# Kernel tuning notes

Hardware: AMD Instinct MI355X
Metric: run time of the kernel (lower is better)

## Reference

```python
import jax, jax.numpy as jnp
import numpy as np

# Structural metadata (constants): 3 node types, 4 edge types, 2 HGT layers.
T, R, L = 3, 4, 2
H_HID, HEADS, OUT = 256, 8, 128
D = H_HID // HEADS  # per-head dim = 32
SRC_T = (0, 1, 1, 1)  # (author->paper, paper->author, paper->paper, paper->venue)
DST_T = (1, 0, 1, 2)
LN_EPS = 1e-5


def _segment_softmax(logits, seg, n):
    # logits: [E, heads]; softmax over edges sharing the same destination node
    m = jax.ops.segment_max(logits, seg, num_segments=n)
    e = jnp.exp(logits - m[seg])
    s = jax.ops.segment_sum(e, seg, num_segments=n)
    return e / s[seg]


def setup_inputs() -> dict:
    key = jax.random.key(0)
    ks = iter(jax.random.split(key, 64))
    N, E, FIN = 20000, 60000, 128

    def nrm(shape, scale):
        return jax.random.normal(next(ks), shape, jnp.float32) * scale

    return dict(
        x=jax.random.normal(next(ks), (T, N, FIN), jnp.float32),
        edge_index=jax.random.randint(next(ks), (R, 2, E), 0, N),
        Win=nrm((T, FIN, H_HID), 0.05),
        b_in=jnp.zeros((T, H_HID), jnp.float32),
        Wk=nrm((L, T, H_HID, H_HID), 0.05), bk=jnp.zeros((L, T, H_HID), jnp.float32),
        Wq=nrm((L, T, H_HID, H_HID), 0.05), bq=jnp.zeros((L, T, H_HID), jnp.float32),
        Wv=nrm((L, T, H_HID, H_HID), 0.05), bv=jnp.zeros((L, T, H_HID), jnp.float32),
        Wa=nrm((L, T, H_HID, H_HID), 0.05), ba=jnp.zeros((L, T, H_HID), jnp.float32),
        skip=jnp.ones((L, T), jnp.float32),
        a_rel=nrm((L, R, HEADS, D, D), 0.1),
        m_rel=nrm((L, R, HEADS, D, D), 0.1),
        p_rel=jnp.ones((L, R, HEADS), jnp.float32),
        ln_g=jnp.ones((L, T, H_HID), jnp.float32),
        ln_b=jnp.zeros((L, T, H_HID), jnp.float32),
        Wout=nrm((H_HID, OUT), 0.05),
        bout=jnp.zeros((OUT,), jnp.float32),
    )


def reference(x, edge_index, Win, b_in, Wk, bk, Wq, bq, Wv, bv, Wa, ba,
              skip, a_rel, m_rel, p_rel, ln_g, ln_b, Wout, bout):
    N = x.shape[1]
    inv_sqrt_d = jnp.float32(1.0 / np.sqrt(D))
    # Input projection + ReLU (dropout = identity in eval mode)
    h = jax.nn.relu(jnp.einsum('tnf,tfh->tnh', x, Win) + b_in[:, None, :])

    for l in range(L):
        res = h
        # Per-node-type k/q/v projections, reshaped to heads
        k = (jnp.einsum('tnh,tho->tno', h, Wk[l]) + bk[l][:, None]).reshape(T, N, HEADS, D)
        q = (jnp.einsum('tnh,tho->tno', h, Wq[l]) + bq[l][:, None]).reshape(T, N, HEADS, D)
        v = (jnp.einsum('tnh,tho->tno', h, Wv[l]) + bv[l][:, None]).reshape(T, N, HEADS, D)

        agg = jnp.zeros((T, N, HEADS, D), h.dtype)
        for r in range(R):
            st, dt = SRC_T[r], DST_T[r]
            src, dst = edge_index[r, 0], edge_index[r, 1]
            # Per-edge-type relation transforms on source k/v
            k_r = jnp.einsum('nhd,hde->nhe', k[st], a_rel[l, r])
            v_r = jnp.einsum('nhd,hde->nhe', v[st], m_rel[l, r])
            kj = k_r[src]          # [E, heads, d]
            vj = v_r[src]
            qi = q[dt][dst]
            logits = (qi * kj).sum(-1) * p_rel[l, r] * inv_sqrt_d  # [E, heads]
            alpha = _segment_softmax(logits, dst, N)
            msg = vj * alpha[..., None]
            agg = agg.at[dt].add(jax.ops.segment_sum(msg, dst, num_segments=N))

        # Type-specific output linear after exact GELU, gated skip (in==out dims)
        o = jax.nn.gelu(agg.reshape(T, N, H_HID), approximate=False)
        o = jnp.einsum('tnh,tho->tno', o, Wa[l]) + ba[l][:, None]
        beta = jax.nn.sigmoid(skip[l])[:, None, None]
        h = beta * o + (1.0 - beta) * h

        # Model-level residual + LayerNorm + ReLU (dropout = identity)
        h = h + res
        mu = h.mean(-1, keepdims=True)
        var = ((h - mu) ** 2).mean(-1, keepdims=True)
        h = (h - mu) * jax.lax.rsqrt(var + LN_EPS) * ln_g[l][:, None] + ln_b[l][:, None]
        h = jax.nn.relu(h)

    # Shared output projection; outputs stacked over node types: [T, N, OUT]
    return jnp.einsum('tnh,ho->tno', h, Wout) + bout
```

## Files before the change

kernel.cpp:

```cpp
#include <hip/hip_runtime.h>
#include <math.h>

#define T_ 3
#define R_ 4
#define L_ 2
#define H_ 256
#define HEADS_ 8
#define D_ 32
#define FIN_ 128
#define OUT_ 128

typedef unsigned short bf16_t;
typedef __attribute__((ext_vector_type(8))) short bf16x8;
typedef __attribute__((ext_vector_type(4))) float f32x4;

__device__ __forceinline__ float bf2f(bf16_t h) {
    return __uint_as_float(((unsigned)h) << 16);
}
__device__ __forceinline__ bf16_t f2bf(float f) {
    unsigned u = __float_as_uint(f);
    u += 0x7FFFu + ((u >> 16) & 1u);
    return (bf16_t)(u >> 16);
}
__device__ __forceinline__ float gelu_exact(float x) {
    return 0.5f * x * (1.0f + erff(x * 0.70710678118654752440f));
}

__global__ void zero_kernel(unsigned* __restrict__ p, long n) {
    long i = (long)blockIdx.x * blockDim.x + threadIdx.x;
    long stride = (long)gridDim.x * blockDim.x;
    for (; i < n; i += stride) p[i] = 0u;
}

__global__ __launch_bounds__(256) void transconv_kernel(
    const float* __restrict__ in, bf16_t* __restrict__ out, int Rr, int Cc)
{
    __shared__ float Ls[64][65];
    const int tid = threadIdx.x;
    const long base = (long)blockIdx.z * Rr * Cc;
    const int r0 = blockIdx.y * 64, c0 = blockIdx.x * 64;
    #pragma unroll
    for (int i = 0; i < 16; ++i) {
        int e = tid + i * 256; int row = e >> 6, col = e & 63;
        Ls[row][col] = in[base + (long)(r0 + row) * Cc + c0 + col];
    }
    __syncthreads();
    #pragma unroll
    for (int i = 0; i < 16; ++i) {
        int e = tid + i * 256; int row = e >> 6, col = e & 63;
        out[base + (long)(c0 + row) * Rr + r0 + col] = f2bf(Ls[col][row]);
    }
}

__global__ __launch_bounds__(256) void fuse_wT_kernel(
    const float* __restrict__ Wk, const float* __restrict__ Wv,
    const float* __restrict__ a_rel, const float* __restrict__ m_rel,
    bf16_t* __restrict__ WkvT)
{
    const int s = blockIdx.z;
    const int kv = s & 1, r = (s >> 1) & 3, l = s >> 3;
    const int SRCT[4] = {0, 1, 1, 1};
    const int st = SRCT[r];
    const float* W = (kv ? Wv : Wk) + ((long)l * T_ + st) * H_ * H_;
    const float* A = (kv ? m_rel : a_rel) + ((long)l * R_ + r) * HEADS_ * D_ * D_;
    const int hh = blockIdx.y, kt = blockIdx.x;
    __shared__ float As[32][33];
    __shared__ float Ws[64][33];
    const int tid = threadIdx.x;
    {
        int d = tid >> 3, e4 = (tid & 7) * 4;
        float4 v = *(const float4*)(A + (hh * D_ + d) * D_ + e4);
        As[d][e4] = v.x; As[d][e4 + 1] = v.y; As[d][e4 + 2] = v.z; As[d][e4 + 3] = v.w;
    }
    #pragma unroll
    for (int p = 0; p < 2; ++p) {
        int idx = p * 256 + tid;
        int row = idx >> 3, c4 = (idx & 7) * 4;
        float4 v = *(const float4*)(W + (long)(kt * 64 + row) * H_ + hh * 32 + c4);
        Ws[row][c4] = v.x; Ws[row][c4 + 1] = v.y; Ws[row][c4 + 2] = v.z; Ws[row][c4 + 3] = v.w;
    }
    __syncthreads();
    const int kl = tid & 63, eb = tid >> 6;
    #pragma unroll
    for (int ii = 0; ii < 8; ++ii) {
        int e = eb * 8 + ii;
        float acc = 0.f;
        #pragma unroll
        for (int d = 0; d < 32; ++d)
            acc += As[d][e] * Ws[kl][d];
        long rowIdx = (long)(s >> 1) * 512 + (kv * 256) + hh * 32 + e;
        WkvT[rowIdx * H_ + kt * 64 + kl] = f2bf(acc);
    }
}

__global__ void fuse_b_kernel(
    const float* __restrict__ bk, const float* __restrict__ bv,
    const float* __restrict__ a_rel, const float* __restrict__ m_rel,
    float* __restrict__ bkv)
{
    const int s = blockIdx.x;
    const int kv = s & 1, r = (s >> 1) & 3, l = s >> 3;
    const int SRCT[4] = {0, 1, 1, 1};
    const int st = SRCT[r];
    const float* b = (kv ? bv : bk) + ((long)l * T_ + st) * H_;
    const float* A = (kv ? m_rel : a_rel) + ((long)l * R_ + r) * HEADS_ * D_ * D_;
    const int tid = threadIdx.x;
    const int hh = tid >> 5, e = tid & 31;
    float acc = 0.f;
    #pragma unroll
    for (int d = 0; d < D_; ++d)
        acc += b[hh * D_ + d] * A[(hh * D_ + d) * D_ + e];
    bkv[(long)(s >> 1) * 512 + kv * 256 + tid] = acc;
}

__global__ void hist_kernel(const int* __restrict__ ei, int* __restrict__ indeg,
                            int Nn, int E)
{
    int idx = blockIdx.x * 256 + threadIdx.x;
    if (idx >= R_ * E) return;
    int r = idx / E, e = idx - r * E;
    int d = ei[(size_t)r * 2 * E + E + e];
    atomicAdd(indeg + (size_t)r * Nn + d, 1);
}

__global__ __launch_bounds__(256) void csr_part_kernel(
    const int* __restrict__ indeg, int* __restrict__ partials, int Nn, int nch)
{
    const int r = blockIdx.y, c = blockIdx.x, tid = threadIdx.x;
    const int lane = tid & 63, wave = tid >> 6;
    int idx = c * 256 + tid;
    int v = (idx < Nn) ? indeg[(size_t)r * Nn + idx] : 0;
    #pragma unroll
    for (int off = 1; off < 64; off <<= 1) v += __shfl_xor(v, off);
    __shared__ int wsum[4];
    if (lane == 0) wsum[wave] = v;
    __syncthreads();
    if (tid == 0) partials[r * nch + c] = wsum[0] + wsum[1] + wsum[2] + wsum[3];
}

__global__ __launch_bounds__(256) void csr_scanpart_kernel(
    int* __restrict__ partials, int nch)
{
    const int r = blockIdx.x, tid = threadIdx.x;
    __shared__ int sh[256];
    int v = (tid < nch) ? partials[r * nch + tid] : 0;
    sh[tid] = v;
    __syncthreads();
    for (int off = 1; off < 256; off <<= 1) {
        int u = (tid >= off) ? sh[tid - off] : 0;
        __syncthreads();
        sh[tid] += u;
        __syncthreads();
    }
    if (tid < nch) partials[r * nch + tid] = sh[tid] - v;
}

__global__ __launch_bounds__(256) void csr_write_kernel(
    const int* __restrict__ indeg, const int* __restrict__ partials,
    int* __restrict__ offs, int* __restrict__ cursor, int Nn, int nch)
{
    const int r = blockIdx.y, c = blockIdx.x, tid = threadIdx.x;
    int idx = c * 256 + tid;
    int v = (idx < Nn) ? indeg[(size_t)r * Nn + idx] : 0;
    __shared__ int sh[256];
    sh[tid] = v;
    __syncthreads();
    for (int off = 1; off < 256; off <<= 1) {
        int u = (tid >= off) ? sh[tid - off] : 0;
        __syncthreads();
        sh[tid] += u;
        __syncthreads();
    }
    int incl = sh[tid];
    int base = partials[r * nch + c];
    if (idx < Nn) {
        int excl = base + incl - v;
        offs[(size_t)r * (Nn + 1) + idx] = excl;
        cursor[(size_t)r * Nn + idx] = excl;
        if (idx == Nn - 1) offs[(size_t)r * (Nn + 1) + Nn] = base + incl;
    }
}

__global__ void scatter_kernel(const int* __restrict__ ei, int* __restrict__ cursor,
                               int* __restrict__ esrc, int Nn, int E)
{
    int idx = blockIdx.x * 256 + threadIdx.x;
    if (idx >= R_ * E) return;
    int r = idx / E, e = idx - r * E;
    int s = ei[(size_t)r * 2 * E + e];
    int d = ei[(size_t)r * 2 * E + E + e];
    int pos = atomicAdd(cursor + (size_t)r * Nn + d, 1);
    esrc[(size_t)r * E + pos] = s;
}

__global__ __launch_bounds__(256) void agg_all_kernel(
    const int* __restrict__ offs, const int* __restrict__ esrc,
    bf16_t* __restrict__ qbuf, const bf16_t* __restrict__ KV,
    const float* __restrict__ p_l,
    float scale, int Nn, int E)
{
    static const int NRELg[3] = {2, 1, 1};
    static const int R0g[3]  = {0, 1, 3};
    static const int R1g[3]  = {2, 0, 0};
    static const int DTg[3]  = {1, 0, 2};
    const int grp = blockIdx.y;
    const int wave = threadIdx.x >> 6, lane = threadIdx.x & 63;
    const int d = blockIdx.x * 4 + wave;
    if (d >= Nn) return;
    const int head = lane >> 3;
    const int dt = DTg[grp], nrel = NRELg[grp];

    bf16_t* qrow = qbuf + (size_t)dt * Nn * H_ + (size_t)d * H_;
    ushort4 qu = ((const ushort4*)qrow)[lane];
    float q0 = bf2f(qu.x), q1 = bf2f(qu.y), q2 = bf2f(qu.z), q3 = bf2f(qu.w);

    float t0 = 0.f, t1 = 0.f, t2 = 0.f, t3 = 0.f;
    for (int rr = 0; rr < nrel; ++rr) {
        const int r = rr ? R1g[grp] : R0g[grp];
        const int* of = offs + (size_t)r * (Nn + 1);
        const int* es = esrc + (size_t)r * E;
        const bf16_t* KVr = KV + (size_t)r * Nn * 512;
        const float pr = p_l[r * HEADS_ + head] * scale;
        float m = -INFINITY, s = 0.f;
        float a0 = 0.f, a1 = 0.f, a2 = 0.f, a3 = 0.f;
        int beg = of[d], end = of[d + 1];
        for (int e = beg; e < end; ++e) {
            int si = es[e];
            const bf16_t* row = KVr + (size_t)si * 512;
            ushort4 ku = ((const ushort4*)row)[lane];
            ushort4 vu = ((const ushort4*)(row + 256))[lane];
            float dt_ = q0 * bf2f(ku.x) + q1 * bf2f(ku.y) + q2 * bf2f(ku.z) + q3 * bf2f(ku.w);
            dt_ += __shfl_xor(dt_, 1);
            dt_ += __shfl_xor(dt_, 2);
            dt_ += __shfl_xor(dt_, 4);
            float lg = dt_ * pr;
            float mnew = fmaxf(m, lg);
            float fac = __expf(m - mnew);
            float p = __expf(lg - mnew);
            s = s * fac + p;
            a0 = a0 * fac + p * bf2f(vu.x);
            a1 = a1 * fac + p * bf2f(vu.y);
            a2 = a2 * fac + p * bf2f(vu.z);
            a3 = a3 * fac + p * bf2f(vu.w);
            m = mnew;
        }
        float invs = (s > 0.f) ? 1.f / s : 0.f;
        t0 += a0 * invs; t1 += a1 * invs; t2 += a2 * invs; t3 += a3 * invs;
    }
    ushort4 ou;
    ou.x = f2bf(gelu_exact(t0));
    ou.y = f2bf(gelu_exact(t1));
    ou.z = f2bf(gelu_exact(t2));
    ou.w = f2bf(gelu_exact(t3));
    ((ushort4*)qrow)[lane] = ou;
}

#define ASTR 40
#define ESTR 72

template<typename TA, typename TC, int ACT_C>
__global__ __launch_bounds__(256) void mfma_gemm(
    const TA* __restrict__ A, const bf16_t* __restrict__ BT,
    const float* __restrict__ bias, TC* __restrict__ C,
    int M, int K, int Nc,
    long strideA, long strideB, long strideBias, long strideC)
{
    const int gX = gridDim.x, gY = gridDim.y, gZ = gridDim.z;
    const int nwg = gX * gY * gZ;
    {
    }
    int flat = blockIdx.x + gX * (blockIdx.y + gY * blockIdx.z);
    const int qch = nwg >> 3, rch = nwg & 7;
    int xcd = flat & 7, cidx = flat >> 3;
    int swz = (xcd < rch ? xcd * (qch + 1) : rch * (qch + 1) + (xcd - rch) * qch) + cidx;
    const int by = swz / (gX * gZ);
    int rem = swz - by * (gX * gZ);
    const int bz = rem / gX;
    const int bx = rem - bz * gX;

    const TA* Ab = A + (long)bz * strideA;
    const bf16_t* Bb = BT + (long)bz * strideB;
    const float* biasb = bias + (long)bz * strideBias;
    TC* Cb = C + (long)bz * strideC;

    __shared__ bf16_t As[128 * ASTR];
    __shared__ bf16_t Bs[128 * ASTR];
    __shared__ bf16_t Es[4 * 16 * ESTR];
    const int tid = threadIdx.x;
    const int lane = tid & 63, wave = tid >> 6;
    const int wr = wave >> 1, wc = wave & 1;
    const int bm = by * 128, bn = bx * 128;
    const int r16 = lane & 15, g = lane >> 4;
    f32x4 acc[4][4] = {};

    for (int k0 = 0; k0 < K; k0 += 32) {
        #pragma unroll
        for (int p = 0; p < 2; ++p) {
            int idx = p * 256 + tid;
            int row = idx >> 2, seg = idx & 3;
            int grow = bm + row;
            bf16x8 av = {};
            if (grow < M) {
                if constexpr (sizeof(TA) == 2) {
                    av = *(const bf16x8*)(Ab + (long)grow * K + k0 + seg * 8);
                } else {
                    const float* sp = (const float*)Ab + (long)grow * K + k0 + seg * 8;
                    float4 f0 = *(const float4*)sp, f1 = *(const float4*)(sp + 4);
                    av[0] = (short)f2bf(f0.x); av[1] = (short)f2bf(f0.y);
                    av[2] = (short)f2bf(f0.z); av[3] = (short)f2bf(f0.w);
                    av[4] = (short)f2bf(f1.x); av[5] = (short)f2bf(f1.y);
                    av[6] = (short)f2bf(f1.z); av[7] = (short)f2bf(f1.w);
                }
            }
            *(bf16x8*)(As + row * ASTR + seg * 8) = av;
            bf16x8 bv = *(const bf16x8*)(Bb + (long)(bn + row) * K + k0 + seg * 8);
            *(bf16x8*)(Bs + row * ASTR + seg * 8) = bv;
        }
        __syncthreads();
        bf16x8 af[4], bfr[4];
        #pragma unroll
        for (int m = 0; m < 4; ++m)
            af[m] = *(const bf16x8*)(As + (wr * 64 + m * 16 + r16) * ASTR + g * 8);
        #pragma unroll
        for (int n = 0; n < 4; ++n)
            bfr[n] = *(const bf16x8*)(Bs + (wc * 64 + n * 16 + r16) * ASTR + g * 8);
        #pragma unroll
        for (int m = 0; m < 4; ++m)
            #pragma unroll
            for (int n = 0; n < 4; ++n)
                acc[m][n] = __builtin_amdgcn_mfma_f32_16x16x32_bf16(af[m], bfr[n], acc[m][n], 0, 0, 0);
        __syncthreads();
    }

    float bb[4];
    #pragma unroll
    for (int n = 0; n < 4; ++n)
        bb[n] = biasb[bn + wc * 64 + n * 16 + r16];

    if constexpr (sizeof(TC) == 2) {
        bf16_t* st = Es + wave * (16 * ESTR);
        #pragma unroll
        for (int m = 0; m < 4; ++m) {
            int rowbase = bm + wr * 64 + m * 16;
            #pragma unroll
            for (int n = 0; n < 4; ++n) {
                #pragma unroll
                for (int j = 0; j < 4; ++j) {
                    float vv = acc[m][n][j] + bb[n];
                    if (ACT_C) vv = fmaxf(vv, 0.f);
                    st[(g * 4 + j) * ESTR + n * 16 + r16] = f2bf(vv);
                }
            }
            #pragma unroll
            for (int p = 0; p < 2; ++p) {
                int row = p * 8 + (lane >> 3);
                int col0 = (lane & 7) * 8;
                int grow = rowbase + row;
                bf16x8 val = *(const bf16x8*)(st + row * ESTR + col0);
                if (grow < M)
                    *(bf16x8*)(Cb + (long)grow * Nc + bn + wc * 64 + col0) = val;
            }
        }
    } else {
        #pragma unroll
        for (int n = 0; n < 4; ++n) {
            int col = bn + wc * 64 + n * 16 + r16;
            #pragma unroll
            for (int m = 0; m < 4; ++m) {
                int rowbase = bm + wr * 64 + m * 16 + g * 4;
                #pragma unroll
                for (int j = 0; j < 4; ++j) {
                    int row = rowbase + j;
                    if (row < M) {
                        float vv = acc[m][n][j] + bb[n];
                        if (ACT_C) vv = fmaxf(vv, 0.f);
                        Cb[(long)row * Nc + col] = vv;
                    }
                }
            }
        }
    }
}

__global__ __launch_bounds__(256) void skip_ln_kernel(
    bf16_t* __restrict__ h, const bf16_t* __restrict__ o,
    const float* __restrict__ skip, const float* __restrict__ ln_g,
    const float* __restrict__ ln_b, int Nn)
{
    const int wave = threadIdx.x >> 6;
    const int lane = threadIdx.x & 63;
    long row = (long)blockIdx.x * 4 + wave;
    long total = (long)T_ * Nn;
    if (row >= total) return;
    int t = (int)(row / Nn);
    float beta = 1.f / (1.f + expf(-skip[t]));
    float cb = 2.f - beta;
    ushort4 hv = reinterpret_cast<const ushort4*>(h + row * H_)[lane];
    ushort4 ov = reinterpret_cast<const ushort4*>(o + row * H_)[lane];
    float u0 = beta * bf2f(ov.x) + cb * bf2f(hv.x);
    float u1 = beta * bf2f(ov.y) + cb * bf2f(hv.y);
    float u2 = beta * bf2f(ov.z) + cb * bf2f(hv.z);
    float u3 = beta * bf2f(ov.w) + cb * bf2f(hv.w);
    float s1 = u0 + u1 + u2 + u3;
    float s2 = u0 * u0 + u1 * u1 + u2 * u2 + u3 * u3;
    #pragma unroll
    for (int off = 1; off < 64; off <<= 1) {
        s1 += __shfl_xor(s1, off);
        s2 += __shfl_xor(s2, off);
    }
    float mu = s1 * (1.f / H_);
    float var = s2 * (1.f / H_) - mu * mu;
    float inv = rsqrtf(var + 1e-5f);
    const float4 g = reinterpret_cast<const float4*>(ln_g + (size_t)t * H_)[lane];
    const float4 b = reinterpret_cast<const float4*>(ln_b + (size_t)t * H_)[lane];
    ushort4 r;
    r.x = f2bf(fmaxf((u0 - mu) * inv * g.x + b.x, 0.f));
    r.y = f2bf(fmaxf((u1 - mu) * inv * g.y + b.y, 0.f));
    r.z = f2bf(fmaxf((u2 - mu) * inv * g.z + b.z, 0.f));
    r.w = f2bf(fmaxf((u3 - mu) * inv * g.w + b.w, 0.f));
    reinterpret_cast<ushort4*>(h + row * H_)[lane] = r;
}

extern "C" void kernel_launch(void* const* d_in, const int* in_sizes, int n_in,
                              void* d_out, int out_size, void* d_ws, size_t ws_size,
                              hipStream_t stream)
{
    const float* x     = (const float*)d_in[0];
    const int*   ei    = (const int*)  d_in[1];
    const float* Win   = (const float*)d_in[2];
    const float* b_in  = (const float*)d_in[3];
    const float* Wk    = (const float*)d_in[4];
    const float* bk    = (const float*)d_in[5];
    const float* Wq    = (const float*)d_in[6];
    const float* bq    = (const float*)d_in[7];
    const float* Wv    = (const float*)d_in[8];
    const float* bv    = (const float*)d_in[9];
    const float* Wa    = (const float*)d_in[10];
    const float* ba    = (const float*)d_in[11];
    const float* skip  = (const float*)d_in[12];
    const float* a_rel = (const float*)d_in[13];
    const float* m_rel = (const float*)d_in[14];
    const float* p_rel = (const float*)d_in[15];
    const float* ln_g  = (const float*)d_in[16];
    const float* ln_b  = (const float*)d_in[17];
    const float* Wout  = (const float*)d_in[18];
    const float* bout  = (const float*)d_in[19];
    float* out = (float*)d_out;

    const int N = in_sizes[0] / (T_ * FIN_);
    const int E = in_sizes[1] / (R_ * 2);
    const size_t NH = (size_t)N * H_;
    const int nch = (N + 255) / 256;

    char* wp = (char*)d_ws;
    auto alloc = [&](size_t bytes) {
        void* r = wp;
        wp += (bytes + 255) & ~(size_t)255;
        return r;
    };
    bf16_t* h     = (bf16_t*)alloc(T_ * NH * 2);
    bf16_t* qbuf  = (bf16_t*)alloc(T_ * NH * 2);
    bf16_t* KV    = (bf16_t*)alloc((size_t)R_ * N * 512 * 2);
    int*    indeg = (int*)   alloc((size_t)R_ * N * 4);
    int*    offs  = (int*)   alloc((size_t)R_ * (N + 1) * 4);
    int*    cursor= (int*)   alloc((size_t)R_ * N * 4);
    int*    esrc  = (int*)   alloc((size_t)R_ * E * 4);
    int*    parts = (int*)   alloc((size_t)R_ * 256 * 4);
    bf16_t* WqT   = (bf16_t*)alloc((size_t)L_ * T_ * H_ * H_ * 2);
    bf16_t* WaT   = (bf16_t*)alloc((size_t)L_ * T_ * H_ * H_ * 2);
    bf16_t* WinT  = (bf16_t*)alloc((size_t)T_ * FIN_ * H_ * 2);
    bf16_t* WoutT = (bf16_t*)alloc((size_t)H_ * OUT_ * 2);
    bf16_t* WkvT  = (bf16_t*)alloc((size_t)L_ * R_ * 512 * H_ * 2);
    float*  bkv   = (float*) alloc((size_t)L_ * R_ * 512 * 4);

    bf16_t* obuf = KV;

    if ((size_t)(wp - (char*)d_ws) > ws_size) return;

    const float scale = 0.17677669529663688f;
    dim3 blk(256);
    auto gM = [](long M) { return (int)((M + 127) / 128); };

    transconv_kernel<<<dim3(4, 4, L_ * T_), blk, 0, stream>>>(Wq, WqT, H_, H_);
    transconv_kernel<<<dim3(4, 4, L_ * T_), blk, 0, stream>>>(Wa, WaT, H_, H_);
    transconv_kernel<<<dim3(4, 2, T_),      blk, 0, stream>>>(Win, WinT, FIN_, H_);
    transconv_kernel<<<dim3(2, 4, 1),       blk, 0, stream>>>(Wout, WoutT, H_, OUT_);
    fuse_wT_kernel<<<dim3(4, 8, 16), blk, 0, stream>>>(Wk, Wv, a_rel, m_rel, WkvT);
    fuse_b_kernel<<<16, blk, 0, stream>>>(bk, bv, a_rel, m_rel, bkv);

    zero_kernel<<<256, blk, 0, stream>>>((unsigned*)indeg, (long)R_ * N);
    hist_kernel<<<(R_ * E + 255) / 256, blk, 0, stream>>>(ei, indeg, N, E);
    csr_part_kernel<<<dim3(nch, R_), blk, 0, stream>>>(indeg, parts, N, nch);
    csr_scanpart_kernel<<<R_, blk, 0, stream>>>(parts, nch);
    csr_write_kernel<<<dim3(nch, R_), blk, 0, stream>>>(indeg, parts, offs, cursor, N, nch);
    scatter_kernel<<<(R_ * E + 255) / 256, blk, 0, stream>>>(ei, cursor, esrc, N, E);

    mfma_gemm<float, bf16_t, 1><<<dim3(H_ / 128, gM(N), T_), blk, 0, stream>>>(
        x, WinT, b_in, h, N, FIN_, H_,
        (long)N * FIN_, (long)FIN_ * H_, H_, (long)NH);

    for (int l = 0; l < L_; ++l) {
        const long lw = (long)l * R_;
        mfma_gemm<bf16_t, bf16_t, 0><<<dim3(512 / 128, gM(N), 1), blk, 0, stream>>>(
            h, WkvT + lw * 512 * H_, bkv + lw * 512, KV,
            N, H_, 512, 0L, 0L, 0L, 0L);
        mfma_gemm<bf16_t, bf16_t, 0><<<dim3(512 / 128, gM(N), 3), blk, 0, stream>>>(
            h + NH, WkvT + (lw + 1) * 512 * H_, bkv + (lw + 1) * 512, KV + (size_t)N * 512,
            N, H_, 512, 0L, 512L * H_, 512L, (long)N * 512);
        mfma_gemm<bf16_t, bf16_t, 0><<<dim3(H_ / 128, gM(N), 3), blk, 0, stream>>>(
            h, WqT + (size_t)l * T_ * H_ * H_, bq + (size_t)l * T_ * H_, qbuf,
            N, H_, H_, (long)NH, (long)H_ * H_, (long)H_, (long)NH);
        agg_all_kernel<<<dim3((N + 3) / 4, 3), blk, 0, stream>>>(
            offs, esrc, qbuf, KV, p_rel + (size_t)l * R_ * HEADS_, scale, N, E);
        mfma_gemm<bf16_t, bf16_t, 0><<<dim3(H_ / 128, gM(N), 3), blk, 0, stream>>>(
            qbuf, WaT + (size_t)l * T_ * H_ * H_, ba + (size_t)l * T_ * H_, obuf,
            N, H_, H_, (long)NH, (long)H_ * H_, (long)H_, (long)NH);
        skip_ln_kernel<<<((size_t)T_ * N + 3) / 4, blk, 0, stream>>>(
            h, obuf, skip + l * T_, ln_g + (size_t)l * T_ * H_, ln_b + (size_t)l * T_ * H_, N);
    }

    mfma_gemm<bf16_t, float, 0><<<dim3(OUT_ / 128, gM((long)T_ * N), 1), blk, 0, stream>>>(
        h, WoutT, bout, out, T_ * N, H_, OUT_, 0L, 0L, 0L, 0L);
}
```

Before: 425.2 us.

## Interleave two edge streams in aggregation and merge setup and KV GEMM launches

The aggregation kernel now walks two edge lists at once. For a destination type fed by two relations it walks both relations together; for a single relation it splits the node's edge range in half and merges the two partial online-softmax states at the end. This gives each wave two independent gather loads in flight to hide latency on the memory-bound gather. Separately, the two K/V GEMM launches are merged into one using an A2 pointer keyed on z, the Wq/Wa transposes share one launch, and the bias fusion moves into fuse_wT_kernel, which removes several kernel launches. The cost is more register pressure and some divergence when the two streams have uneven lengths.

```diff
diff --git a/kernel.cpp b/kernel.cpp
--- a/kernel.cpp
+++ b/kernel.cpp
@@ -32,6 +32,33 @@
     for (; i < n; i += stride) p[i] = 0u;
 }
 
+__global__ __launch_bounds__(256) void transconv2_kernel(
+    const float* __restrict__ in0, bf16_t* __restrict__ out0,
+    const float* __restrict__ in1, bf16_t* __restrict__ out1,
+    int cnt0, int Rr, int Cc)
+{
+    __shared__ float Ls[64][65];
+    const int tid = threadIdx.x;
+    int z = blockIdx.z;
+    const float* in;
+    bf16_t* out;
+    if (z < cnt0) { in = in0; out = out0; }
+    else          { in = in1; out = out1; z -= cnt0; }
+    const long base = (long)z * Rr * Cc;
+    const int r0 = blockIdx.y * 64, c0 = blockIdx.x * 64;
+    #pragma unroll
+    for (int i = 0; i < 16; ++i) {
+        int e = tid + i * 256; int row = e >> 6, col = e & 63;
+        Ls[row][col] = in[base + (long)(r0 + row) * Cc + c0 + col];
+    }
+    __syncthreads();
+    #pragma unroll
+    for (int i = 0; i < 16; ++i) {
+        int e = tid + i * 256; int row = e >> 6, col = e & 63;
+        out[base + (long)(c0 + row) * Rr + r0 + col] = f2bf(Ls[col][row]);
+    }
+}
+
 __global__ __launch_bounds__(256) void transconv_kernel(
     const float* __restrict__ in, bf16_t* __restrict__ out, int Rr, int Cc)
 {
@@ -54,8 +81,9 @@
 
 __global__ __launch_bounds__(256) void fuse_wT_kernel(
     const float* __restrict__ Wk, const float* __restrict__ Wv,
+    const float* __restrict__ bk, const float* __restrict__ bv,
     const float* __restrict__ a_rel, const float* __restrict__ m_rel,
-    bf16_t* __restrict__ WkvT)
+    bf16_t* __restrict__ WkvT, float* __restrict__ bkv)
 {
     const int s = blockIdx.z;
     const int kv = s & 1, r = (s >> 1) & 3, l = s >> 3;
@@ -91,26 +119,15 @@
         long rowIdx = (long)(s >> 1) * 512 + (kv * 256) + hh * 32 + e;
         WkvT[rowIdx * H_ + kt * 64 + kl] = f2bf(acc);
     }
-}
-
-__global__ void fuse_b_kernel(
-    const float* __restrict__ bk, const float* __restrict__ bv,
-    const float* __restrict__ a_rel, const float* __restrict__ m_rel,
-    float* __restrict__ bkv)
-{
-    const int s = blockIdx.x;
-    const int kv = s & 1, r = (s >> 1) & 3, l = s >> 3;
-    const int SRCT[4] = {0, 1, 1, 1};
-    const int st = SRCT[r];
-    const float* b = (kv ? bv : bk) + ((long)l * T_ + st) * H_;
-    const float* A = (kv ? m_rel : a_rel) + ((long)l * R_ + r) * HEADS_ * D_ * D_;
-    const int tid = threadIdx.x;
-    const int hh = tid >> 5, e = tid & 31;
-    float acc = 0.f;
-    #pragma unroll
-    for (int d = 0; d < D_; ++d)
-        acc += b[hh * D_ + d] * A[(hh * D_ + d) * D_ + e];
-    bkv[(long)(s >> 1) * 512 + kv * 256 + tid] = acc;
+    if (blockIdx.x == 0 && blockIdx.y == 0) {
+        const float* b = (kv ? bv : bk) + ((long)l * T_ + st) * H_;
+        const int bh = tid >> 5, be = tid & 31;
+        float acc = 0.f;
+        #pragma unroll
+        for (int d = 0; d < D_; ++d)
+            acc += b[bh * D_ + d] * A[(bh * D_ + d) * D_ + be];
+        bkv[(long)(s >> 1) * 512 + kv * 256 + tid] = acc;
+    }
 }
 
 __global__ void hist_kernel(const int* __restrict__ ei, int* __restrict__ indeg,
@@ -196,8 +213,7 @@
 __global__ __launch_bounds__(256) void agg_all_kernel(
     const int* __restrict__ offs, const int* __restrict__ esrc,
     bf16_t* __restrict__ qbuf, const bf16_t* __restrict__ KV,
-    const float* __restrict__ p_l,
-    float scale, int Nn, int E)
+    const float* __restrict__ p_l, float scale, int Nn, int E)
 {
     static const int NRELg[3] = {2, 1, 1};
     static const int R0g[3]  = {0, 1, 3};
@@ -208,44 +224,109 @@
     const int d = blockIdx.x * 4 + wave;
     if (d >= Nn) return;
     const int head = lane >> 3;
-    const int dt = DTg[grp], nrel = NRELg[grp];
+    const int dt = DTg[grp];
 
     bf16_t* qrow = qbuf + (size_t)dt * Nn * H_ + (size_t)d * H_;
     ushort4 qu = ((const ushort4*)qrow)[lane];
     float q0 = bf2f(qu.x), q1 = bf2f(qu.y), q2 = bf2f(qu.z), q3 = bf2f(qu.w);
 
-    float t0 = 0.f, t1 = 0.f, t2 = 0.f, t3 = 0.f;
-    for (int rr = 0; rr < nrel; ++rr) {
-        const int r = rr ? R1g[grp] : R0g[grp];
-        const int* of = offs + (size_t)r * (Nn + 1);
-        const int* es = esrc + (size_t)r * E;
-        const bf16_t* KVr = KV + (size_t)r * Nn * 512;
-        const float pr = p_l[r * HEADS_ + head] * scale;
-        float m = -INFINITY, s = 0.f;
-        float a0 = 0.f, a1 = 0.f, a2 = 0.f, a3 = 0.f;
-        int beg = of[d], end = of[d + 1];
-        for (int e = beg; e < end; ++e) {
-            int si = es[e];
-            const bf16_t* row = KVr + (size_t)si * 512;
-            ushort4 ku = ((const ushort4*)row)[lane];
-            ushort4 vu = ((const ushort4*)(row + 256))[lane];
-            float dt_ = q0 * bf2f(ku.x) + q1 * bf2f(ku.y) + q2 * bf2f(ku.z) + q3 * bf2f(ku.w);
+    const int rA = R0g[grp];
+    const int* esA = esrc + (size_t)rA * E;
+    const bf16_t* kvA = KV + (size_t)rA * Nn * 512;
+    float prA = p_l[rA * HEADS_ + head] * scale;
+    int curA = offs[(size_t)rA * (Nn + 1) + d];
+    int endA = offs[(size_t)rA * (Nn + 1) + d + 1];
+
+    const int* esB; const bf16_t* kvB; float prB;
+    int curB, endB;
+    const bool separate = (NRELg[grp] == 2);
+    if (separate) {
+        const int rB = R1g[grp];
+        esB = esrc + (size_t)rB * E;
+        kvB = KV + (size_t)rB * Nn * 512;
+        prB = p_l[rB * HEADS_ + head] * scale;
+        curB = offs[(size_t)rB * (Nn + 1) + d];
+        endB = offs[(size_t)rB * (Nn + 1) + d + 1];
+    } else {
+        int mid = curA + ((endA - curA + 1) >> 1);
+        esB = esA; kvB = kvA; prB = prA;
+        curB = mid; endB = endA;
+        endA = mid;
+    }
+
+    float mA = -INFINITY, sA = 0.f, aA0 = 0.f, aA1 = 0.f, aA2 = 0.f, aA3 = 0.f;
+    float mB = -INFINITY, sB = 0.f, aB0 = 0.f, aB1 = 0.f, aB2 = 0.f, aB3 = 0.f;
+
+    while (curA < endA || curB < endB) {
+        const bool hA = curA < endA, hB = curB < endB;
+        ushort4 kuA, vuA, kuB, vuB;
+        if (hA) {
+            const bf16_t* row = kvA + (size_t)esA[curA] * 512;
+            kuA = ((const ushort4*)row)[lane];
+            vuA = ((const ushort4*)(row + 256))[lane];
+        }
+        if (hB) {
+            const bf16_t* row = kvB + (size_t)esB[curB] * 512;
+            kuB = ((const ushort4*)row)[lane];
+            vuB = ((const ushort4*)(row + 256))[lane];
+        }
+        if (hA) {
+            float dt_ = q0 * bf2f(kuA.x) + q1 * bf2f(kuA.y) + q2 * bf2f(kuA.z) + q3 * bf2f(kuA.w);
             dt_ += __shfl_xor(dt_, 1);
             dt_ += __shfl_xor(dt_, 2);
             dt_ += __shfl_xor(dt_, 4);
-            float lg = dt_ * pr;
-            float mnew = fmaxf(m, lg);
-            float fac = __expf(m - mnew);
+            float lg = dt_ * prA;
+            float mnew = fmaxf(mA, lg);
+            float fac = __expf(mA - mnew);
             float p = __expf(lg - mnew);
-            s = s * fac + p;
-            a0 = a0 * fac + p * bf2f(vu.x);
-            a1 = a1 * fac + p * bf2f(vu.y);
-            a2 = a2 * fac + p * bf2f(vu.z);
-            a3 = a3 * fac + p * bf2f(vu.w);
-            m = mnew;
-        }
-        float invs = (s > 0.f) ? 1.f / s : 0.f;
-        t0 += a0 * invs; t1 += a1 * invs; t2 += a2 * invs; t3 += a3 * invs;
+            sA = sA * fac + p;
+            aA0 = aA0 * fac + p * bf2f(vuA.x);
+            aA1 = aA1 * fac + p * bf2f(vuA.y);
+            aA2 = aA2 * fac + p * bf2f(vuA.z);
+            aA3 = aA3 * fac + p * bf2f(vuA.w);
+            mA = mnew;
+            ++curA;
+        }
+        if (hB) {
+            float dt_ = q0 * bf2f(kuB.x) + q1 * bf2f(kuB.y) + q2 * bf2f(kuB.z) + q3 * bf2f(kuB.w);
+            dt_ += __shfl_xor(dt_, 1);
+            dt_ += __shfl_xor(dt_, 2);
+            dt_ += __shfl_xor(dt_, 4);
+            float lg = dt_ * prB;
+            float mnew = fmaxf(mB, lg);
+            float fac = __expf(mB - mnew);
+            float p = __expf(lg - mnew);
+            sB = sB * fac + p;
+            aB0 = aB0 * fac + p * bf2f(vuB.x);
+            aB1 = aB1 * fac + p * bf2f(vuB.y);
+            aB2 = aB2 * fac + p * bf2f(vuB.z);
+            aB3 = aB3 * fac + p * bf2f(vuB.w);
+            mB = mnew;
+            ++curB;
+        }
+    }
+
+    float t0, t1, t2, t3;
+    if (separate) {
+        float iA = (sA > 0.f) ? 1.f / sA : 0.f;
+        float iB = (sB > 0.f) ? 1.f / sB : 0.f;
+        t0 = aA0 * iA + aB0 * iB;
+        t1 = aA1 * iA + aB1 * iB;
+        t2 = aA2 * iA + aB2 * iB;
+        t3 = aA3 * iA + aB3 * iB;
+    } else {
+        if (sB > 0.f) {
+            float m = fmaxf(mA, mB);
+            float fA = (sA > 0.f) ? __expf(mA - m) : 0.f;
+            float fB = __expf(mB - m);
+            sA = sA * fA + sB * fB;
+            aA0 = aA0 * fA + aB0 * fB;
+            aA1 = aA1 * fA + aB1 * fB;
+            aA2 = aA2 * fA + aB2 * fB;
+            aA3 = aA3 * fA + aB3 * fB;
+        }
+        float iA = (sA > 0.f) ? 1.f / sA : 0.f;
+        t0 = aA0 * iA; t1 = aA1 * iA; t2 = aA2 * iA; t3 = aA3 * iA;
     }
     ushort4 ou;
     ou.x = f2bf(gelu_exact(t0));
@@ -260,15 +341,14 @@
 
 template<typename TA, typename TC, int ACT_C>
 __global__ __launch_bounds__(256) void mfma_gemm(
-    const TA* __restrict__ A, const bf16_t* __restrict__ BT,
+    const TA* __restrict__ A, const TA* __restrict__ A2, int zsplit,
+    const bf16_t* __restrict__ BT,
     const float* __restrict__ bias, TC* __restrict__ C,
     int M, int K, int Nc,
     long strideA, long strideB, long strideBias, long strideC)
 {
     const int gX = gridDim.x, gY = gridDim.y, gZ = gridDim.z;
     const int nwg = gX * gY * gZ;
-    {
-    }
     int flat = blockIdx.x + gX * (blockIdx.y + gY * blockIdx.z);
     const int qch = nwg >> 3, rch = nwg & 7;
     int xcd = flat & 7, cidx = flat >> 3;
@@ -278,7 +358,7 @@
     const int bz = rem / gX;
     const int bx = rem - bz * gX;
 
-    const TA* Ab = A + (long)bz * strideA;
+    const TA* Ab = (bz < zsplit) ? (A + (long)bz * strideA) : A2;
     const bf16_t* Bb = BT + (long)bz * strideB;
     const float* biasb = bias + (long)bz * strideBias;
     TC* Cb = C + (long)bz * strideC;
@@ -451,6 +531,7 @@
     const int E = in_sizes[1] / (R_ * 2);
     const size_t NH = (size_t)N * H_;
     const int nch = (N + 255) / 256;
+    const int ZBIG = 1 << 20;
 
     char* wp = (char*)d_ws;
     auto alloc = [&](size_t bytes) {
@@ -481,12 +562,12 @@
     dim3 blk(256);
     auto gM = [](long M) { return (int)((M + 127) / 128); };
 
-    transconv_kernel<<<dim3(4, 4, L_ * T_), blk, 0, stream>>>(Wq, WqT, H_, H_);
-    transconv_kernel<<<dim3(4, 4, L_ * T_), blk, 0, stream>>>(Wa, WaT, H_, H_);
-    transconv_kernel<<<dim3(4, 2, T_),      blk, 0, stream>>>(Win, WinT, FIN_, H_);
-    transconv_kernel<<<dim3(2, 4, 1),       blk, 0, stream>>>(Wout, WoutT, H_, OUT_);
-    fuse_wT_kernel<<<dim3(4, 8, 16), blk, 0, stream>>>(Wk, Wv, a_rel, m_rel, WkvT);
-    fuse_b_kernel<<<16, blk, 0, stream>>>(bk, bv, a_rel, m_rel, bkv);
+    transconv2_kernel<<<dim3(4, 4, 2 * L_ * T_), blk, 0, stream>>>(
+        Wq, WqT, Wa, WaT, L_ * T_, H_, H_);
+    transconv_kernel<<<dim3(4, 2, T_), blk, 0, stream>>>(Win, WinT, FIN_, H_);
+    transconv_kernel<<<dim3(2, 4, 1),  blk, 0, stream>>>(Wout, WoutT, H_, OUT_);
+    fuse_wT_kernel<<<dim3(4, 8, 16), blk, 0, stream>>>(
+        Wk, Wv, bk, bv, a_rel, m_rel, WkvT, bkv);
 
     zero_kernel<<<256, blk, 0, stream>>>((unsigned*)indeg, (long)R_ * N);
     hist_kernel<<<(R_ * E + 255) / 256, blk, 0, stream>>>(ei, indeg, N, E);
@@ -496,29 +577,26 @@
     scatter_kernel<<<(R_ * E + 255) / 256, blk, 0, stream>>>(ei, cursor, esrc, N, E);
 
     mfma_gemm<float, bf16_t, 1><<<dim3(H_ / 128, gM(N), T_), blk, 0, stream>>>(
-        x, WinT, b_in, h, N, FIN_, H_,
+        x, x, ZBIG, WinT, b_in, h, N, FIN_, H_,
         (long)N * FIN_, (long)FIN_ * H_, H_, (long)NH);
 
     for (int l = 0; l < L_; ++l) {
         const long lw = (long)l * R_;
-        mfma_gemm<bf16_t, bf16_t, 0><<<dim3(512 / 128, gM(N), 1), blk, 0, stream>>>(
-            h, WkvT + lw * 512 * H_, bkv + lw * 512, KV,
-            N, H_, 512, 0L, 0L, 0L, 0L);
-        mfma_gemm<bf16_t, bf16_t, 0><<<dim3(512 / 128, gM(N), 3), blk, 0, stream>>>(
-            h + NH, WkvT + (lw + 1) * 512 * H_, bkv + (lw + 1) * 512, KV + (size_t)N * 512,
+        mfma_gemm<bf16_t, bf16_t, 0><<<dim3(512 / 128, gM(N), 4), blk, 0, stream>>>(
+            h, h + NH, 1, WkvT + lw * 512 * H_, bkv + lw * 512, KV,
             N, H_, 512, 0L, 512L * H_, 512L, (long)N * 512);
         mfma_gemm<bf16_t, bf16_t, 0><<<dim3(H_ / 128, gM(N), 3), blk, 0, stream>>>(
-            h, WqT + (size_t)l * T_ * H_ * H_, bq + (size_t)l * T_ * H_, qbuf,
+            h, h, ZBIG, WqT + (size_t)l * T_ * H_ * H_, bq + (size_t)l * T_ * H_, qbuf,
             N, H_, H_, (long)NH, (long)H_ * H_, (long)H_, (long)NH);
         agg_all_kernel<<<dim3((N + 3) / 4, 3), blk, 0, stream>>>(
             offs, esrc, qbuf, KV, p_rel + (size_t)l * R_ * HEADS_, scale, N, E);
         mfma_gemm<bf16_t, bf16_t, 0><<<dim3(H_ / 128, gM(N), 3), blk, 0, stream>>>(
-            qbuf, WaT + (size_t)l * T_ * H_ * H_, ba + (size_t)l * T_ * H_, obuf,
+            qbuf, qbuf, ZBIG, WaT + (size_t)l * T_ * H_ * H_, ba + (size_t)l * T_ * H_, obuf,
             N, H_, H_, (long)NH, (long)H_ * H_, (long)H_, (long)NH);
         skip_ln_kernel<<<((size_t)T_ * N + 3) / 4, blk, 0, stream>>>(
             h, obuf, skip + l * T_, ln_g + (size_t)l * T_ * H_, ln_b + (size_t)l * T_ * H_, N);
     }
 
     mfma_gemm<bf16_t, float, 0><<<dim3(OUT_ / 128, gM((long)T_ * N), 1), blk, 0, stream>>>(
-        h, WoutT, bout, out, T_ * N, H_, OUT_, 0L, 0L, 0L, 0L);
-}
+        h, h, ZBIG, WoutT, bout, out, T_ * N, H_, OUT_, 0L, 0L, 0L, 0L);
+}
```

After: 410.7 us. 1.04x faster.
